# Kernel tuning notes

Hardware: AMD Instinct MI355X
Metric: run time of the kernel (lower is better)

## Reference

```python
import jax, jax.numpy as jnp
import numpy as np

LN_EPS = 1e-5  # nn.LayerNorm default (module's self.eps is unused by LayerNorm)


def setup_inputs() -> dict:
    key = jax.random.key(0)
    ks = jax.random.split(key, 5)
    B, L, H, OUT = 64, 16384, 128, 128
    x = jax.random.normal(ks[0], (B, L, 2), dtype=jnp.float32)
    W1 = jax.random.normal(ks[1], (2, H), dtype=jnp.float32) * (1.0 / np.sqrt(2))
    b1 = jnp.zeros((H,), dtype=jnp.float32)
    W2 = jax.random.normal(ks[2], (H, H), dtype=jnp.float32) * (1.0 / np.sqrt(H))
    b2 = jnp.zeros((H,), dtype=jnp.float32)
    Wh = jax.random.normal(ks[3], (2 * H, OUT), dtype=jnp.float32) * (1.0 / np.sqrt(2 * H))
    bh = jnp.zeros((OUT,), dtype=jnp.float32)
    gamma = jnp.ones((OUT,), dtype=jnp.float32)
    beta = jnp.zeros((OUT,), dtype=jnp.float32)
    return {"x": x, "W1": W1, "b1": b1, "W2": W2, "b2": b2,
            "Wh": Wh, "bh": bh, "gamma": gamma, "beta": beta}


def reference(x, W1, b1, W2, b2, Wh, bh, gamma, beta):
    # x: [B, L, 2]
    dx = jnp.roll(x, shift=-1, axis=1) - x          # edge diffs [B, L, 2]
    h = jax.nn.gelu(dx @ W1 + b1, approximate=False)  # [B, L, H]
    h = jax.nn.gelu(h @ W2 + b2, approximate=False)   # [B, L, H]
    h_mean = h.mean(axis=1)                          # [B, H]
    h_max = h.max(axis=1)                            # [B, H]
    z = jnp.concatenate([h_mean, h_max], axis=-1) @ Wh + bh  # [B, OUT]
    mu = z.mean(axis=-1, keepdims=True)
    var = z.var(axis=-1, keepdims=True)
    return (z - mu) * jax.lax.rsqrt(var + LN_EPS) * gamma + beta
```

## Files before the change

### kernel.cpp

```cpp
#include <hip/hip_runtime.h>
#include <hip/hip_bf16.h>
#include <hip/hip_fp16.h>

#define L_LEN 16384
#define NB 64
#define NCHUNK 32
#define CHUNK 512

typedef short bf16x8 __attribute__((ext_vector_type(8)));
typedef float f32x4 __attribute__((ext_vector_type(4)));
typedef unsigned int u32x4 __attribute__((ext_vector_type(4)));

__device__ __forceinline__ unsigned short f2bf(float f) {
    unsigned u = __float_as_uint(f);
    return (unsigned short)((u + 0x7FFFu + ((u >> 16) & 1u)) >> 16);
}

__device__ __forceinline__ unsigned cvt_pk_bf16(float lo, float hi) {
    unsigned r;
    asm("v_cvt_pk_bf16_f32 %0, %1, %2" : "=v"(r) : "v"(lo), "v"(hi));
    return r;
}

__device__ __forceinline__ float gelu_s(float x) {
    float x2 = x * x;
    float f  = x * fmaf(-0.1029437f, x2, -2.30220789f);
    float e  = __builtin_amdgcn_exp2f(f);
    return x * __builtin_amdgcn_rcpf(1.0f + e);
}

__global__ __launch_bounds__(256) void k0_prep(const float* __restrict__ W2,
                                               unsigned short* __restrict__ w2t,
                                               float2* __restrict__ gtab) {
    if (blockIdx.x < 64) {
        int i = blockIdx.x * 256 + threadIdx.x;
        int n = i >> 7, k = i & 127;
        w2t[i] = f2bf(W2[k * 128 + n]);
    } else {
        for (int e = threadIdx.x; e < 512; e += 256) {
            double x0 = (double)e * (1.0 / 32.0) - 8.0;
            double x1 = x0 + (1.0 / 32.0);
            double g0 = 0.5 * x0 * (1.0 + erf(x0 * 0.7071067811865476));
            double g1 = 0.5 * x1 * (1.0 + erf(x1 * 0.7071067811865476));
            double s  = (g1 - g0) * 32.0;
            double v  = g0 - s * x0;
            gtab[e] = make_float2((float)v, (float)s);
        }
    }
}

__global__ __launch_bounds__(256) void k1_fused(
    const float* __restrict__ x,
    const float* __restrict__ W1,
    const float* __restrict__ b1,
    const unsigned short* __restrict__ w2t,
    const float2* __restrict__ gtab,
    const float* __restrict__ b2,
    float* __restrict__ psum,
    float* __restrict__ pmaxf)
{
    __shared__ char   sW[32768];
    __shared__ float2 sTab[512];
    __shared__ float  sW1f[256];
    __shared__ float  sb1f[128];

    const int tid  = threadIdx.x;
    const int b    = blockIdx.x >> 5;
    const int c    = blockIdx.x & 31;
    const int lane = tid & 63;
    const int w    = tid >> 6;
    const int lr   = lane & 15;
    const int lk   = lane >> 4;
    const int swz  = (lr & 7) << 4;

    {
        const float4* src = (const float4*)w2t;
        #pragma unroll
        for (int it = 0; it < 8; ++it) {
            int cch = tid + it * 256;
            int dst = (cch << 4) ^ (((cch >> 4) & 7) << 4);
            *(float4*)(sW + dst) = src[cch];
        }
    }
    {
        float4 v = ((const float4*)gtab)[tid];
        *(float4*)&sTab[tid * 2] = v;
    }
    if (tid < 128) {
        sW1f[tid]       = W1[tid];
        sW1f[128 + tid] = W1[128 + tid];
        sb1f[tid]       = b1[tid];
    }
    __syncthreads();

    float b2r[8];
    #pragma unroll
    for (int nt = 0; nt < 8; ++nt) b2r[nt] = b2[nt * 16 + lr];

    float runS[8], runM[8];
    #pragma unroll
    for (int nt = 0; nt < 8; ++nt) { runS[nt] = 0.0f; runM[nt] = -3.0e38f; }

    const float2* xr  = (const float2*)x + (size_t)b * L_LEN;
    const int     tk0 = c * CHUNK + w * 128;

    const float* w0base = sW1f + lk * 8;
    const float* w1base = sW1f + 128 + lk * 8;
    const float* bbase  = sb1f + lk * 8;

    #define GELU_LUT(p, out) {                                          \
        float xm_ = __builtin_amdgcn_fmed3f((p), -8.0f, 7.96875f);      \
        float t_  = fmaf(xm_, 32.0f, 256.0f);                           \
        int   i_  = (int)t_;                                            \
        float2 vs_ = sTab[i_];                                          \
        (out) = fmaf(vs_.y, (p), vs_.x);                                \
    }

    for (int it = 0; it < 4; ++it) {
        #pragma unroll
        for (int rb = 0; rb < 2; ++rb) {
            int g = tk0 + it * 32 + rb * 16 + lr;
            float2 a0 = xr[g];
            int gn = (g + 1) & (L_LEN - 1);
            float2 a1 = xr[gn];
            float dx0 = a1.x - a0.x, dx1 = a1.y - a0.y;

            f32x4 acc[8];
            #pragma unroll
            for (int nt = 0; nt < 8; ++nt) acc[nt] = (f32x4){0.f, 0.f, 0.f, 0.f};

            #pragma unroll
            for (int kt = 0; kt < 4; ++kt) {
                float4 w0a = *(const float4*)(w0base + kt * 32);
                float4 w0b = *(const float4*)(w0base + kt * 32 + 4);
                float4 w1a = *(const float4*)(w1base + kt * 32);
                float4 w1b = *(const float4*)(w1base + kt * 32 + 4);
                float4 ba  = *(const float4*)(bbase  + kt * 32);
                float4 bb  = *(const float4*)(bbase  + kt * 32 + 4);

                float h[8];
                #pragma unroll
                for (int j = 0; j < 4; ++j) {
                    float p = fmaf(dx0, w0a[j], fmaf(dx1, w1a[j], ba[j]));
                    GELU_LUT(p, h[j]);
                }
                #pragma unroll
                for (int j = 0; j < 4; ++j) {
                    float p = fmaf(dx0, w0b[j], fmaf(dx1, w1b[j], bb[j]));
                    GELU_LUT(p, h[4 + j]);
                }

                union { u32x4 u; bf16x8 v; } cv;
                cv.u = (u32x4){cvt_pk_bf16(h[0], h[1]), cvt_pk_bf16(h[2], h[3]),
                               cvt_pk_bf16(h[4], h[5]), cvt_pk_bf16(h[6], h[7])};
                bf16x8 aF = cv.v;

                #pragma unroll
                for (int nt = 0; nt < 8; ++nt) {
                    int bo = ((nt * 16 + lr) << 8) + kt * 64 + (lk << 4);
                    bo ^= swz;
                    bf16x8 bF = *(const bf16x8*)(sW + bo);
                    acc[nt] = __builtin_amdgcn_mfma_f32_16x16x32_bf16(aF, bF, acc[nt], 0, 0, 0);
                }
            }

            #pragma unroll
            for (int nt = 0; nt < 8; ++nt) {
                float v0 = gelu_s(acc[nt][0] + b2r[nt]);
                float v1 = gelu_s(acc[nt][1] + b2r[nt]);
                float v2 = gelu_s(acc[nt][2] + b2r[nt]);
                float v3 = gelu_s(acc[nt][3] + b2r[nt]);
                runS[nt] += (v0 + v1) + (v2 + v3);
                runM[nt] = fmaxf(fmaxf(fmaxf(v0, v1), fmaxf(v2, v3)), runM[nt]);
            }
        }
    }

    #pragma unroll
    for (int nt = 0; nt < 8; ++nt) {
        float s = runS[nt];
        s += __shfl_xor(s, 16, 64);
        s += __shfl_xor(s, 32, 64);
        float m = runM[nt];
        m = fmaxf(m, __shfl_xor(m, 16, 64));
        m = fmaxf(m, __shfl_xor(m, 32, 64));
        runS[nt] = s;
        runM[nt] = m;
    }

    __syncthreads();
    float* scrS = (float*)sW;
    float* scrM = (float*)(sW + 2048);
    if (lk == 0) {
        #pragma unroll
        for (int nt = 0; nt < 8; ++nt) {
            scrS[w * 128 + nt * 16 + lr] = runS[nt];
            scrM[w * 128 + nt * 16 + lr] = runM[nt];
        }
    }
    __syncthreads();
    if (tid < 128) {
        float s = (scrS[tid] + scrS[128 + tid]) + (scrS[256 + tid] + scrS[384 + tid]);
        float m = fmaxf(fmaxf(scrM[tid], scrM[128 + tid]), fmaxf(scrM[256 + tid], scrM[384 + tid]));
        int o = (b * NCHUNK + c) * 128 + tid;
        psum[o]  = s;
        pmaxf[o] = m;
    }
}

__global__ __launch_bounds__(128) void k2_final(
    const float* __restrict__ psum,
    const float* __restrict__ pmaxf,
    const float* __restrict__ Wh,
    const float* __restrict__ bh,
    const float* __restrict__ gamma,
    const float* __restrict__ beta,
    float* __restrict__ out)
{
    __shared__ float cat[256];
    __shared__ float red[4];
    const int b = blockIdx.x, f = threadIdx.x;
    float s = 0.0f, m = -3.0e38f;
    #pragma unroll
    for (int c = 0; c < NCHUNK; ++c) {
        int o = (b * NCHUNK + c) * 128 + f;
        s += psum[o];
        m = fmaxf(m, pmaxf[o]);
    }
    cat[f]       = s * (1.0f / 16384.0f);
    cat[128 + f] = m;
    __syncthreads();

    float z = bh[f];
    #pragma unroll 4
    for (int j = 0; j < 256; ++j) z = fmaf(cat[j], Wh[j * 128 + f], z);

    float s1 = z, s2 = z * z;
    #pragma unroll
    for (int off = 32; off >= 1; off >>= 1) {
        s1 += __shfl_xor(s1, off, 64);
        s2 += __shfl_xor(s2, off, 64);
    }
    int lane = f & 63, wv = f >> 6;
    if (lane == 0) { red[wv] = s1; red[2 + wv] = s2; }
    __syncthreads();
    float S1 = red[0] + red[1], S2 = red[2] + red[3];
    float mu  = S1 * (1.0f / 128.0f);
    float var = S2 * (1.0f / 128.0f) - mu * mu;
    out[b * 128 + f] = (z - mu) * rsqrtf(var + 1e-5f) * gamma[f] + beta[f];
}

extern "C" void kernel_launch(void* const* d_in, const int* in_sizes, int n_in,
                              void* d_out, int out_size, void* d_ws, size_t ws_size,
                              hipStream_t stream) {
    const float* x     = (const float*)d_in[0];
    const float* W1    = (const float*)d_in[1];
    const float* b1    = (const float*)d_in[2];
    const float* W2    = (const float*)d_in[3];
    const float* b2    = (const float*)d_in[4];
    const float* Wh    = (const float*)d_in[5];
    const float* bh    = (const float*)d_in[6];
    const float* gamma = (const float*)d_in[7];
    const float* beta  = (const float*)d_in[8];
    float* out = (float*)d_out;

    char* wsb = (char*)d_ws;
    unsigned short* w2t = (unsigned short*)wsb;
    float2* gtab = (float2*)(wsb + 32768);
    float* psum  = (float*)(wsb + 36864);
    float* pmaxf = (float*)(wsb + 36864 + NB * NCHUNK * 128 * 4);

    k0_prep<<<65, 256, 0, stream>>>(W2, w2t, gtab);
    k1_fused<<<NB * NCHUNK, 256, 0, stream>>>(x, W1, b1, w2t, gtab, b2, psum, pmaxf);
    k2_final<<<NB, 128, 0, stream>>>(psum, pmaxf, Wh, bh, gamma, beta, out);
}
```

Measured before the change: 107.4 us.

## Restructure MLP inner loop to share W2 fragments across two row blocks

Both 16-row blocks' layer-1 GELU A-fragments are now computed up front, and the loop is reordered so each W2 B-fragment loaded from LDS feeds two MFMAs, one per row block. This halves the LDS reads of W2 and interleaves independent MFMA chains. The b2 bias is folded into the accumulator initialisation, and the swizzled address base is precomputed. In exchange, register pressure rises from holding eight A-fragments and two accumulators per output tile, which could lower occupancy.

New measurement: 123.7 us. +15.1%, slower.

```diff
diff --git a/kernel.cpp b/kernel.cpp
--- a/kernel.cpp
+++ b/kernel.cpp
@@ -108,6 +108,8 @@
     const float* w1base = sW1f + 128 + lk * 8;
     const float* bbase  = sb1f + lk * 8;
 
+    const int vb = (lr << 8) | (lk << 4);
+
     #define GELU_LUT(p, out) {                                          \
         float xm_ = __builtin_amdgcn_fmed3f((p), -8.0f, 7.96875f);      \
         float t_  = fmaf(xm_, 32.0f, 256.0f);                           \
@@ -116,63 +118,80 @@
         (out) = fmaf(vs_.y, (p), vs_.x);                                \
     }
 
-    for (int it = 0; it < 4; ++it) {
-        #pragma unroll
-        for (int rb = 0; rb < 2; ++rb) {
-            int g = tk0 + it * 32 + rb * 16 + lr;
-            float2 a0 = xr[g];
-            int gn = (g + 1) & (L_LEN - 1);
-            float2 a1 = xr[gn];
-            float dx0 = a1.x - a0.x, dx1 = a1.y - a0.y;
-
-            f32x4 acc[8];
-            #pragma unroll
-            for (int nt = 0; nt < 8; ++nt) acc[nt] = (f32x4){0.f, 0.f, 0.f, 0.f};
-
+    for (int body = 0; body < 4; ++body) {
+        const int T0 = tk0 + body * 32;
+        int g0 = T0 + lr;
+        int g1 = T0 + 16 + lr;
+        float2 a00 = xr[g0], a01 = xr[(g0 + 1) & (L_LEN - 1)];
+        float2 a10 = xr[g1], a11 = xr[(g1 + 1) & (L_LEN - 1)];
+        float dxA0 = a01.x - a00.x, dxA1 = a01.y - a00.y;
+        float dxB0 = a11.x - a10.x, dxB1 = a11.y - a10.y;
+
+        bf16x8 aF0[4], aF1[4];
+        #pragma unroll
+        for (int kt = 0; kt < 4; ++kt) {
+            float4 w0a = *(const float4*)(w0base + kt * 32);
+            float4 w0b = *(const float4*)(w0base + kt * 32 + 4);
+            float4 w1a = *(const float4*)(w1base + kt * 32);
+            float4 w1b = *(const float4*)(w1base + kt * 32 + 4);
+            float4 ba  = *(const float4*)(bbase  + kt * 32);
+            float4 bb  = *(const float4*)(bbase  + kt * 32 + 4);
+
+            float h[8];
+            #pragma unroll
+            for (int j = 0; j < 4; ++j) {
+                float p = fmaf(dxA0, w0a[j], fmaf(dxA1, w1a[j], ba[j]));
+                GELU_LUT(p, h[j]);
+            }
+            #pragma unroll
+            for (int j = 0; j < 4; ++j) {
+                float p = fmaf(dxA0, w0b[j], fmaf(dxA1, w1b[j], bb[j]));
+                GELU_LUT(p, h[4 + j]);
+            }
+            union { u32x4 u; bf16x8 v; } cv0;
+            cv0.u = (u32x4){cvt_pk_bf16(h[0], h[1]), cvt_pk_bf16(h[2], h[3]),
+                            cvt_pk_bf16(h[4], h[5]), cvt_pk_bf16(h[6], h[7])};
+            aF0[kt] = cv0.v;
+
+            #pragma unroll
+            for (int j = 0; j < 4; ++j) {
+                float p = fmaf(dxB0, w0a[j], fmaf(dxB1, w1a[j], ba[j]));
+                GELU_LUT(p, h[j]);
+            }
+            #pragma unroll
+            for (int j = 0; j < 4; ++j) {
+                float p = fmaf(dxB0, w0b[j], fmaf(dxB1, w1b[j], bb[j]));
+                GELU_LUT(p, h[4 + j]);
+            }
+            union { u32x4 u; bf16x8 v; } cv1;
+            cv1.u = (u32x4){cvt_pk_bf16(h[0], h[1]), cvt_pk_bf16(h[2], h[3]),
+                            cvt_pk_bf16(h[4], h[5]), cvt_pk_bf16(h[6], h[7])};
+            aF1[kt] = cv1.v;
+        }
+
+        #pragma unroll
+        for (int nt = 0; nt < 8; ++nt) {
+            f32x4 acc0 = (f32x4){b2r[nt], b2r[nt], b2r[nt], b2r[nt]};
+            f32x4 acc1 = acc0;
             #pragma unroll
             for (int kt = 0; kt < 4; ++kt) {
-                float4 w0a = *(const float4*)(w0base + kt * 32);
-                float4 w0b = *(const float4*)(w0base + kt * 32 + 4);
-                float4 w1a = *(const float4*)(w1base + kt * 32);
-                float4 w1b = *(const float4*)(w1base + kt * 32 + 4);
-                float4 ba  = *(const float4*)(bbase  + kt * 32);
-                float4 bb  = *(const float4*)(bbase  + kt * 32 + 4);
-
-                float h[8];
-                #pragma unroll
-                for (int j = 0; j < 4; ++j) {
-                    float p = fmaf(dx0, w0a[j], fmaf(dx1, w1a[j], ba[j]));
-                    GELU_LUT(p, h[j]);
-                }
-                #pragma unroll
-                for (int j = 0; j < 4; ++j) {
-                    float p = fmaf(dx0, w0b[j], fmaf(dx1, w1b[j], bb[j]));
-                    GELU_LUT(p, h[4 + j]);
-                }
-
-                union { u32x4 u; bf16x8 v; } cv;
-                cv.u = (u32x4){cvt_pk_bf16(h[0], h[1]), cvt_pk_bf16(h[2], h[3]),
-                               cvt_pk_bf16(h[4], h[5]), cvt_pk_bf16(h[6], h[7])};
-                bf16x8 aF = cv.v;
-
-                #pragma unroll
-                for (int nt = 0; nt < 8; ++nt) {
-                    int bo = ((nt * 16 + lr) << 8) + kt * 64 + (lk << 4);
-                    bo ^= swz;
-                    bf16x8 bF = *(const bf16x8*)(sW + bo);
-                    acc[nt] = __builtin_amdgcn_mfma_f32_16x16x32_bf16(aF, bF, acc[nt], 0, 0, 0);
-                }
-            }
-
-            #pragma unroll
-            for (int nt = 0; nt < 8; ++nt) {
-                float v0 = gelu_s(acc[nt][0] + b2r[nt]);
-                float v1 = gelu_s(acc[nt][1] + b2r[nt]);
-                float v2 = gelu_s(acc[nt][2] + b2r[nt]);
-                float v3 = gelu_s(acc[nt][3] + b2r[nt]);
-                runS[nt] += (v0 + v1) + (v2 + v3);
-                runM[nt] = fmaxf(fmaxf(fmaxf(v0, v1), fmaxf(v2, v3)), runM[nt]);
-            }
+                int bo = (vb + kt * 64) ^ swz;
+                bf16x8 bF = *(const bf16x8*)(sW + bo + nt * 4096);
+                acc0 = __builtin_amdgcn_mfma_f32_16x16x32_bf16(aF0[kt], bF, acc0, 0, 0, 0);
+                acc1 = __builtin_amdgcn_mfma_f32_16x16x32_bf16(aF1[kt], bF, acc1, 0, 0, 0);
+            }
+            float v0 = gelu_s(acc0[0]);
+            float v1 = gelu_s(acc0[1]);
+            float v2 = gelu_s(acc0[2]);
+            float v3 = gelu_s(acc0[3]);
+            float v4 = gelu_s(acc1[0]);
+            float v5 = gelu_s(acc1[1]);
+            float v6 = gelu_s(acc1[2]);
+            float v7 = gelu_s(acc1[3]);
+            runS[nt] += ((v0 + v1) + (v2 + v3)) + ((v4 + v5) + (v6 + v7));
+            float m0 = fmaxf(fmaxf(v0, v1), fmaxf(v2, v3));
+            float m1 = fmaxf(fmaxf(v4, v5), fmaxf(v6, v7));
+            runM[nt] = fmaxf(runM[nt], fmaxf(m0, m1));
         }
     }
 
```
